# Kernel tuning notes

Measured on AMD Instinct MI355X. Metric: run time of the kernel, lower is better.

The kernel has to match this reference:

```python
import jax, jax.numpy as jnp
import numpy as np

N = 50000      # nodes
E = 800000     # edges (before self-loops)
IN_DIM = 256
HID = 32       # per-head hidden of conv1
OUT = 8        # per-head out of conv2 (mean over heads)
H = 4          # heads


def setup_inputs() -> dict:
    key = jax.random.key(0)
    k = jax.random.split(key, 8)
    x = jax.random.normal(k[0], (N, IN_DIM), dtype=jnp.float32)
    src = jax.random.randint(k[1], (E,), 0, N)
    dst = jax.random.randint(k[2], (E,), 0, N)
    # emulate remove_self_loops: perturb any accidental self-loop
    dst = jnp.where(src == dst, (dst + 1) % N, dst)
    edge_index = jnp.stack([src, dst])
    sc1 = 1.0 / np.sqrt(IN_DIM)
    W1 = jax.random.uniform(k[3], (IN_DIM, H * HID), jnp.float32, -sc1, sc1)
    att1 = jax.random.uniform(k[4], (H, HID), jnp.float32, -0.1, 0.1)
    b1 = jnp.zeros((H * HID,), jnp.float32)
    sc2 = 1.0 / np.sqrt(H * HID)
    W2 = jax.random.uniform(k[5], (H * HID, H * OUT), jnp.float32, -sc2, sc2)
    att2 = jax.random.uniform(k[6], (H, OUT), jnp.float32, -0.1, 0.1)
    b2 = jnp.zeros((OUT,), jnp.float32)
    return {"x": x, "edge_index": edge_index, "W1": W1, "att1": att1,
            "b1": b1, "W2": W2, "att2": att2, "b2": b2}


def _segment_softmax(logits, seg, num_segments):
    # logits: [E, H], seg: [E] destination ids. Every segment is non-empty
    # (self-loops added), so no -inf survives.
    m = jnp.full((num_segments, logits.shape[1]), -jnp.inf, logits.dtype)
    m = m.at[seg].max(logits)
    e = jnp.exp(logits - m[seg])
    z = jax.ops.segment_sum(e, seg, num_segments=num_segments)
    return e / (z[seg] + 1e-16)


def _oodgat_conv(x, W, att, bias, src, dst, concat):
    n = x.shape[0]
    h = (x @ W).reshape(n, att.shape[0], att.shape[1])          # [N, H, C]
    s = jax.nn.sigmoid(jnp.einsum('nhc,hc->nh', h, att))        # [N, H] node scores
    si, sj = s[dst], s[src]                                      # [E, H]
    # OODGAT similarity weight (adjust=True): agree-in-distribution term
    logits = si * sj + (1.0 - si) * (1.0 - sj)
    alpha = _segment_softmax(logits, dst, n)                     # [E, H]
    msg = h[src] * alpha[:, :, None]                             # [E, H, C]
    out = jax.ops.segment_sum(msg, dst, num_segments=n)          # [N, H, C]
    out = out.reshape(n, -1) if concat else out.mean(axis=1)
    return out + bias


def reference(x, edge_index, W1, att1, b1, W2, att2, b2):
    n = x.shape[0]
    loop = jnp.arange(n)
    src = jnp.concatenate([edge_index[0], loop])  # add_self_loops
    dst = jnp.concatenate([edge_index[1], loop])
    # eval mode: dropout (drop_input/drop_prob/drop_edge) are identity
    h = jax.nn.elu(_oodgat_conv(x, W1, att1, b1, src, dst, True))
    return _oodgat_conv(h, W2, att2, b2, src, dst, False)
```

## Files before the change

### kernel.cpp

```cpp
#include <hip/hip_runtime.h>
#include <math.h>


typedef __attribute__((ext_vector_type(8))) short bf16x8;
typedef __attribute__((ext_vector_type(4))) float f32x4;

__device__ inline ushort f2bf(float f) {
    uint u = __float_as_uint(f);
    return (ushort)((u + 0x7fffu + ((u >> 16) & 1u)) >> 16);
}
__device__ inline float bf_lo(uint u) { return __uint_as_float(u << 16); }
__device__ inline float bf_hi(uint u) { return __uint_as_float(u & 0xffff0000u); }


__global__ void count_pos_k(const int* __restrict__ dstA, int E, int ET,
                            int* __restrict__ deg, ushort* __restrict__ epos) {
    int e = blockIdx.x * blockDim.x + threadIdx.x;
    if (e >= ET) return;
    int d = (e < E) ? dstA[e] : (e - E);
    epos[e] = (ushort)atomicAdd(&deg[d], 1);
}

__global__ __launch_bounds__(256) void scan_a_k(const int* __restrict__ deg, int n,
                                                int* __restrict__ rowstart,
                                                int* __restrict__ bsum) {
    __shared__ int ts[256];
    int t = threadIdx.x;
    int idx = blockIdx.x * 1024 + t * 4;
    int4 v = make_int4(0, 0, 0, 0);
    if (idx + 3 < n) {
        v = *(const int4*)(deg + idx);
    } else {
        if (idx < n)     v.x = deg[idx];
        if (idx + 1 < n) v.y = deg[idx + 1];
        if (idx + 2 < n) v.z = deg[idx + 2];
        if (idx + 3 < n) v.w = deg[idx + 3];
    }
    int s = v.x + v.y + v.z + v.w;
    ts[t] = s;
    __syncthreads();
#pragma unroll
    for (int off = 1; off < 256; off <<= 1) {
        int u = (t >= off) ? ts[t - off] : 0;
        __syncthreads();
        ts[t] += u;
        __syncthreads();
    }
    int excl = ts[t] - s;
    int p1 = excl + v.x, p2 = p1 + v.y, p3 = p2 + v.z;
    if (idx < n)     rowstart[idx]     = excl;
    if (idx + 1 < n) rowstart[idx + 1] = p1;
    if (idx + 2 < n) rowstart[idx + 2] = p2;
    if (idx + 3 < n) rowstart[idx + 3] = p3;
    if (t == 255) bsum[blockIdx.x] = ts[255];
}

__global__ __launch_bounds__(256) void scan_b_k(const int* __restrict__ bsum, int nb,
                                                int* __restrict__ boff,
                                                int* __restrict__ totalp) {
    __shared__ int ts[256];
    int t = threadIdx.x;
    int v = (t < nb) ? bsum[t] : 0;
    ts[t] = v;
    __syncthreads();
#pragma unroll
    for (int off = 1; off < 256; off <<= 1) {
        int u = (t >= off) ? ts[t - off] : 0;
        __syncthreads();
        ts[t] += u;
        __syncthreads();
    }
    if (t < nb) boff[t] = ts[t] - v;
    if (t == nb - 1) *totalp = ts[t];
}

__global__ void scan_c_k(int* __restrict__ rowstart, const int* __restrict__ boff,
                         int n) {
    int i = blockIdx.x * blockDim.x + threadIdx.x;
    if (i < n) rowstart[i] += boff[i >> 10];
}

__global__ void scatter_k(const int* __restrict__ srcA, const int* __restrict__ dstA,
                          int E, int ET, const int* __restrict__ rowstart,
                          const ushort* __restrict__ epos,
                          ushort* __restrict__ csrc) {
    int e = blockIdx.x * blockDim.x + threadIdx.x;
    if (e >= ET) return;
    int d, s;
    if (e < E) { d = dstA[e]; s = srcA[e]; } else { d = e - E; s = e - E; }
    csrc[rowstart[d] + epos[e]] = (ushort)s;
}


__global__ void prep_wt_k(const float* __restrict__ W, ushort* __restrict__ Wt) {
    int idx = blockIdx.x * blockDim.x + threadIdx.x;
    if (idx >= 256 * 128) return;
    int k = idx >> 7, col = idx & 127;
    Wt[col * 256 + k] = f2bf(W[idx]);
}


__global__ __launch_bounds__(256) void gemm1_k(const float* __restrict__ X,
                                               const ushort* __restrict__ Wt,
                                               const float* __restrict__ ATT1,
                                               uint* __restrict__ H1b,
                                               float* __restrict__ S1, int n) {
    __shared__ __align__(16) ushort Alds[4][128][8];
    __shared__ __align__(16) ushort Blds[4][128][8];
    __shared__ float att1s[128];
    int tid = threadIdx.x;
    int wid = tid >> 6;
    int lane = tid & 63;
    int g = lane >> 4;
    int lr = lane & 15;
    int brow = blockIdx.x * 128;
    if (tid < 128) att1s[tid] = ATT1[tid];

    f32x4 acc[2][8];
#pragma unroll
    for (int rt = 0; rt < 2; ++rt)
#pragma unroll
        for (int ct = 0; ct < 8; ++ct) acc[rt][ct] = (f32x4){0.f, 0.f, 0.f, 0.f};

    for (int k0 = 0; k0 < 256; k0 += 32) {
#pragma unroll
        for (int rep = 0; rep < 2; ++rep) {
            int idx = tid + rep * 256;
            int r = idx >> 2, koct = idx & 3;
            int gr = brow + r;
            float4 a0, a1;
            if (gr < n) {
                const float* p = X + (size_t)gr * 256 + k0 + koct * 8;
                a0 = *(const float4*)p;
                a1 = *(const float4*)(p + 4);
            } else {
                a0 = a1 = make_float4(0.f, 0.f, 0.f, 0.f);
            }
            uint4 pk;
            pk.x = (uint)f2bf(a0.x) | ((uint)f2bf(a0.y) << 16);
            pk.y = (uint)f2bf(a0.z) | ((uint)f2bf(a0.w) << 16);
            pk.z = (uint)f2bf(a1.x) | ((uint)f2bf(a1.y) << 16);
            pk.w = (uint)f2bf(a1.z) | ((uint)f2bf(a1.w) << 16);
            *(uint4*)&Alds[koct][r][0] = pk;
        }
#pragma unroll
        for (int rep = 0; rep < 2; ++rep) {
            int idx = tid + rep * 256;
            int col = idx & 127, koct = idx >> 7;
            *(uint4*)&Blds[koct][col][0] =
                *(const uint4*)(Wt + (size_t)col * 256 + k0 + koct * 8);
        }
        __syncthreads();
        bf16x8 xf0 = *(bf16x8*)&Alds[g][wid * 32 + lr][0];
        bf16x8 xf1 = *(bf16x8*)&Alds[g][wid * 32 + 16 + lr][0];
#pragma unroll
        for (int ct = 0; ct < 8; ++ct) {
            bf16x8 wf = *(bf16x8*)&Blds[g][ct * 16 + lr][0];
            acc[0][ct] = __builtin_amdgcn_mfma_f32_16x16x32_bf16(wf, xf0, acc[0][ct], 0, 0, 0);
            acc[1][ct] = __builtin_amdgcn_mfma_f32_16x16x32_bf16(wf, xf1, acc[1][ct], 0, 0, 0);
        }
        __syncthreads();
    }
#pragma unroll
    for (int rt = 0; rt < 2; ++rt) {
        int row = brow + wid * 32 + rt * 16 + lr;
        if (row < n) {
#pragma unroll
            for (int ct = 0; ct < 8; ++ct) {
                uint lo = (uint)f2bf(acc[rt][ct][0]) | ((uint)f2bf(acc[rt][ct][1]) << 16);
                uint hi = (uint)f2bf(acc[rt][ct][2]) | ((uint)f2bf(acc[rt][ct][3]) << 16);
                *(uint2*)(H1b + (size_t)row * 64 + ct * 8 + g * 2) = make_uint2(lo, hi);
            }
        }
        float sc[4] = {0.f, 0.f, 0.f, 0.f};
#pragma unroll
        for (int ct = 0; ct < 8; ++ct) {
            int base = ct * 16 + g * 4;
#pragma unroll
            for (int j = 0; j < 4; ++j)
                sc[ct >> 1] = fmaf(acc[rt][ct][j], att1s[base + j], sc[ct >> 1]);
        }
#pragma unroll
        for (int h = 0; h < 4; ++h) {
            sc[h] += __shfl_xor(sc[h], 16);
            sc[h] += __shfl_xor(sc[h], 32);
        }
        if (g == 0 && row < n) {
            float4 sv;
            sv.x = 1.f / (1.f + __expf(-sc[0]));
            sv.y = 1.f / (1.f + __expf(-sc[1]));
            sv.z = 1.f / (1.f + __expf(-sc[2]));
            sv.w = 1.f / (1.f + __expf(-sc[3]));
            *(float4*)(S1 + (size_t)row * 4) = sv;
        }
    }
}


__global__ __launch_bounds__(512, 8) void conv1_k(const uint* __restrict__ H1b,
                                                  const float* __restrict__ S1,
                                                  const int* __restrict__ rowstart,
                                                  const ushort* __restrict__ csrc,
                                                  const float* __restrict__ b1,
                                                  const float* __restrict__ W2,
                                                  const float* __restrict__ ATT2,
                                                  ushort* __restrict__ H2b,
                                                  float* __restrict__ S2,
                                                  int n, int nwaves) {
    __shared__ float w2t[32][132];
    __shared__ float rowbuf[8][128];
    __shared__ float wbuf[8][64][4];
    __shared__ float att2s[32];
    int tid = threadIdx.x;
    for (int idx = tid; idx < 4096; idx += 512) {
        int k = idx >> 5, c = idx & 31;
        w2t[c][k] = W2[idx];
    }
    if (tid < 32) att2s[tid] = ATT2[tid];
    __syncthreads();

    int wid = tid >> 6;
    int lane = tid & 63;
    int hd = lane >> 4;
    int half = lane >> 5, cc2 = lane & 31;
    int gwave = blockIdx.x * 8 + wid;
    float2 b1v = *(const float2*)(b1 + lane * 2);

    for (int dst = gwave; dst < n; dst += nwaves) {
        int rs = rowstart[dst], re = rowstart[dst + 1];
        float4 si4 = *(const float4*)(S1 + (size_t)dst * 4);
        float z0 = 0.f, z1 = 0.f, z2 = 0.f, z3 = 0.f;
        float x0 = 0.f, x1 = 0.f, x2 = 0.f, x3 = 0.f;
        float y0 = 0.f, y1 = 0.f, y2 = 0.f, y3 = 0.f;

        for (int cb = rs; cb < re; cb += 64) {
            int cc = min(64, re - cb);
            int sv = 0;
            if (lane < cc) {
                sv = csrc[cb + lane];
                float4 sj = *(const float4*)(S1 + (size_t)sv * 4);
                float w0 = __expf(fmaf(si4.x, sj.x, (1.f - si4.x) * (1.f - sj.x)));
                float w1 = __expf(fmaf(si4.y, sj.y, (1.f - si4.y) * (1.f - sj.y)));
                float w2 = __expf(fmaf(si4.z, sj.z, (1.f - si4.z) * (1.f - sj.z)));
                float w3 = __expf(fmaf(si4.w, sj.w, (1.f - si4.w) * (1.f - sj.w)));
                *(float4*)&wbuf[wid][lane][0] = make_float4(w0, w1, w2, w3);
            }
            asm volatile("s_waitcnt lgkmcnt(0)" ::: "memory");
            int e = 0;
            for (; e + 7 < cc; e += 8) {
                int sA = __builtin_amdgcn_readlane(sv, e);
                int sB = __builtin_amdgcn_readlane(sv, e + 1);
                int sC = __builtin_amdgcn_readlane(sv, e + 2);
                int sD = __builtin_amdgcn_readlane(sv, e + 3);
                int sE = __builtin_amdgcn_readlane(sv, e + 4);
                int sF = __builtin_amdgcn_readlane(sv, e + 5);
                int sG = __builtin_amdgcn_readlane(sv, e + 6);
                int sH = __builtin_amdgcn_readlane(sv, e + 7);
                float wA = wbuf[wid][e][hd],     wB = wbuf[wid][e + 1][hd];
                float wC = wbuf[wid][e + 2][hd], wD = wbuf[wid][e + 3][hd];
                float wE = wbuf[wid][e + 4][hd], wF = wbuf[wid][e + 5][hd];
                float wG = wbuf[wid][e + 6][hd], wH = wbuf[wid][e + 7][hd];
                uint uA = H1b[(size_t)sA * 64 + lane];
                uint uB = H1b[(size_t)sB * 64 + lane];
                uint uC = H1b[(size_t)sC * 64 + lane];
                uint uD = H1b[(size_t)sD * 64 + lane];
                uint uE = H1b[(size_t)sE * 64 + lane];
                uint uF = H1b[(size_t)sF * 64 + lane];
                uint uG = H1b[(size_t)sG * 64 + lane];
                uint uH = H1b[(size_t)sH * 64 + lane];
                z0 += wA + wE; z1 += wB + wF; z2 += wC + wG; z3 += wD + wH;
                x0 = fmaf(wA, bf_lo(uA), x0); x1 = fmaf(wB, bf_lo(uB), x1);
                x2 = fmaf(wC, bf_lo(uC), x2); x3 = fmaf(wD, bf_lo(uD), x3);
                x0 = fmaf(wE, bf_lo(uE), x0); x1 = fmaf(wF, bf_lo(uF), x1);
                x2 = fmaf(wG, bf_lo(uG), x2); x3 = fmaf(wH, bf_lo(uH), x3);
                y0 = fmaf(wA, bf_hi(uA), y0); y1 = fmaf(wB, bf_hi(uB), y1);
                y2 = fmaf(wC, bf_hi(uC), y2); y3 = fmaf(wD, bf_hi(uD), y3);
                y0 = fmaf(wE, bf_hi(uE), y0); y1 = fmaf(wF, bf_hi(uF), y1);
                y2 = fmaf(wG, bf_hi(uG), y2); y3 = fmaf(wH, bf_hi(uH), y3);
            }
            for (; e < cc; ++e) {
                int s = __builtin_amdgcn_readlane(sv, e);
                float w = wbuf[wid][e][hd];
                uint u = H1b[(size_t)s * 64 + lane];
                z0 += w;
                x0 = fmaf(w, bf_lo(u), x0);
                y0 = fmaf(w, bf_hi(u), y0);
            }
            asm volatile("" ::: "memory");
        }
        float inv = 1.f / ((z0 + z1) + (z2 + z3) + 1e-16f);
        float r0 = ((x0 + x1) + (x2 + x3)) * inv + b1v.x;
        float r1 = ((y0 + y1) + (y2 + y3)) * inv + b1v.y;
        r0 = (r0 > 0.f) ? r0 : (__expf(r0) - 1.f);
        r1 = (r1 > 0.f) ? r1 : (__expf(r1) - 1.f);

        *(float2*)&rowbuf[wid][lane * 2] = make_float2(r0, r1);
        asm volatile("s_waitcnt lgkmcnt(0)" ::: "memory");
        const float* rb = &rowbuf[wid][half * 64];
        const float* wr = &w2t[cc2][half * 64];
        float sum = 0.f;
#pragma unroll
        for (int k = 0; k < 64; k += 4) {
            float4 rv = *(const float4*)(rb + k);
            float4 wv = *(const float4*)(wr + k);
            sum = fmaf(rv.x, wv.x, sum);
            sum = fmaf(rv.y, wv.y, sum);
            sum = fmaf(rv.z, wv.z, sum);
            sum = fmaf(rv.w, wv.w, sum);
        }
        sum += __shfl_xor(sum, 32);
        if (half == 0) H2b[(size_t)dst * 32 + cc2] = f2bf(sum);

        float v = sum * att2s[cc2];
        v += __shfl_xor(v, 1);
        v += __shfl_xor(v, 2);
        v += __shfl_xor(v, 4);
        if (half == 0 && (cc2 & 7) == 0)
            S2[dst * 4 + (cc2 >> 3)] = 1.f / (1.f + __expf(-v));
    }
}


__global__ __launch_bounds__(256, 8) void conv2_k(const uint* __restrict__ H2u,
                                                  const float* __restrict__ S,
                                                  const int* __restrict__ rowstart,
                                                  const ushort* __restrict__ csrc,
                                                  const float* __restrict__ b2,
                                                  float* __restrict__ Out,
                                                  int n, int nwaves) {
    int gwave = (int)((blockIdx.x * blockDim.x + threadIdx.x) >> 6);
    int lane = threadIdx.x & 63;
    int eslot = lane >> 4;
    int c2 = lane & 15;
    int hd = c2 >> 2;
    float2 b2v;
    b2v.x = b2[2 * (c2 & 3)];
    b2v.y = b2[2 * (c2 & 3) + 1];

    for (int dst = gwave; dst < n; dst += nwaves) {
        float si = S[dst * 4 + hd];
        float omsi = 1.f - si;
        int rs = rowstart[dst], re = rowstart[dst + 1];
        int cnt = re - rs;
        float z = 0.f, x = 0.f, y = 0.f;
        int i = eslot;
        for (; i + 4 < cnt; i += 8) {
            int s0 = csrc[rs + i];
            int s1 = csrc[rs + i + 4];
            float sj0 = S[s0 * 4 + hd];
            float sj1 = S[s1 * 4 + hd];
            uint u0 = H2u[(size_t)s0 * 16 + c2];
            uint u1 = H2u[(size_t)s1 * 16 + c2];
            float w0 = __expf(fmaf(si, sj0, omsi * (1.f - sj0)));
            float w1 = __expf(fmaf(si, sj1, omsi * (1.f - sj1)));
            z += w0 + w1;
            x = fmaf(w0, bf_lo(u0), x); x = fmaf(w1, bf_lo(u1), x);
            y = fmaf(w0, bf_hi(u0), y); y = fmaf(w1, bf_hi(u1), y);
        }
        if (i < cnt) {
            int s0 = csrc[rs + i];
            float sj0 = S[s0 * 4 + hd];
            uint u0 = H2u[(size_t)s0 * 16 + c2];
            float w0 = __expf(fmaf(si, sj0, omsi * (1.f - sj0)));
            z += w0;
            x = fmaf(w0, bf_lo(u0), x);
            y = fmaf(w0, bf_hi(u0), y);
        }
        z += __shfl_xor(z, 16); z += __shfl_xor(z, 32);
        x += __shfl_xor(x, 16); x += __shfl_xor(x, 32);
        y += __shfl_xor(y, 16); y += __shfl_xor(y, 32);
        float inv = 1.f / (z + 1e-16f);
        float r0 = x * inv, r1 = y * inv;
        r0 += __shfl_xor(r0, 4, 16); r0 += __shfl_xor(r0, 8, 16);
        r1 += __shfl_xor(r1, 4, 16); r1 += __shfl_xor(r1, 8, 16);
        if (eslot == 0 && c2 < 4) {
            float2 o = make_float2(r0 * 0.25f + b2v.x, r1 * 0.25f + b2v.y);
            *(float2*)(Out + (size_t)dst * 8 + 2 * c2) = o;
        }
    }
}


static inline size_t align16(size_t x) { return (x + 15) & ~(size_t)15; }

extern "C" void kernel_launch(void* const* d_in, const int* in_sizes, int n_in,
                              void* d_out, int out_size, void* d_ws, size_t ws_size,
                              hipStream_t stream) {
    const float* x    = (const float*)d_in[0];
    const int*   edge = (const int*)d_in[1];
    const float* W1   = (const float*)d_in[2];
    const float* att1 = (const float*)d_in[3];
    const float* b1   = (const float*)d_in[4];
    const float* W2   = (const float*)d_in[5];
    const float* att2 = (const float*)d_in[6];
    const float* b2   = (const float*)d_in[7];

    int N  = in_sizes[0] / 256;
    int E  = in_sizes[1] / 2;
    int ET = E + N;
    int NB = (N + 1023) / 1024;
    const int* srcA = edge;
    const int* dstA = edge + E;

    char* ws = (char*)d_ws;
    uint*  h1b  = (uint*)ws;   ws += align16((size_t)N * 64 * sizeof(uint));
    ushort* h2b = (ushort*)ws; ws += align16((size_t)N * 32 * sizeof(ushort));
    float* s1   = (float*)ws;  ws += align16((size_t)N * 4 * sizeof(float));
    float* s2   = (float*)ws;  ws += align16((size_t)N * 4 * sizeof(float));
    int* rowstart = (int*)ws;  ws += align16((size_t)(N + 1) * sizeof(int));
    int* deg      = (int*)ws;  ws += align16((size_t)N * sizeof(int));
    ushort* csrc  = (ushort*)ws; ws += align16((size_t)ET * sizeof(ushort));
    ushort* epos  = (ushort*)ws; ws += align16((size_t)ET * sizeof(ushort));
    int* bsum     = (int*)ws;  ws += align16((size_t)NB * sizeof(int));
    int* boff     = (int*)ws;  ws += align16((size_t)NB * sizeof(int));
    ushort* w1t   = (ushort*)ws; ws += align16((size_t)256 * 128 * sizeof(ushort));

    hipMemsetAsync(deg, 0, (size_t)N * sizeof(int), stream);

    int eb = (ET + 255) / 256;
    count_pos_k<<<eb, 256, 0, stream>>>(dstA, E, ET, deg, epos);
    scan_a_k<<<NB, 256, 0, stream>>>(deg, N, rowstart, bsum);
    scan_b_k<<<1, 256, 0, stream>>>(bsum, NB, boff, rowstart + N);
    scan_c_k<<<(N + 255) / 256, 256, 0, stream>>>(rowstart, boff, N);
    scatter_k<<<eb, 256, 0, stream>>>(srcA, dstA, E, ET, rowstart, epos, csrc);

    prep_wt_k<<<(256 * 128 + 255) / 256, 256, 0, stream>>>(W1, w1t);
    gemm1_k<<<(N + 127) / 128, 256, 0, stream>>>(x, w1t, att1, h1b, s1, N);

    int c1_blocks = 1024;
    if (c1_blocks > (N + 7) / 8) c1_blocks = (N + 7) / 8;
    int c1_waves = c1_blocks * 8;
    conv1_k<<<c1_blocks, 512, 0, stream>>>(h1b, s1, rowstart, csrc, b1, W2, att2,
                                           h2b, s2, N, c1_waves);

    int c2_blocks = 2048;
    if (c2_blocks > (N + 3) / 4) c2_blocks = (N + 3) / 4;
    int c2_waves = c2_blocks * 4;
    conv2_k<<<c2_blocks, 256, 0, stream>>>((const uint*)h2b, s2, rowstart, csrc, b2,
                                           (float*)d_out, N, c2_waves);
}
```

Before: 154.8 us.

## Vectorize CSR build kernels, use contiguous dst ranges, precompute conv2 edge weights

```diff
diff --git a/kernel.cpp b/kernel.cpp
--- a/kernel.cpp
+++ b/kernel.cpp
@@ -15,10 +15,26 @@
 
 __global__ void count_pos_k(const int* __restrict__ dstA, int E, int ET,
                             int* __restrict__ deg, ushort* __restrict__ epos) {
-    int e = blockIdx.x * blockDim.x + threadIdx.x;
-    if (e >= ET) return;
-    int d = (e < E) ? dstA[e] : (e - E);
-    epos[e] = (ushort)atomicAdd(&deg[d], 1);
+    int e4 = (blockIdx.x * blockDim.x + threadIdx.x) * 4;
+    if (e4 >= ET) return;
+    if (e4 + 3 < E) {
+        int4 d = *(const int4*)(dstA + e4);
+        ushort4 p;
+        p.x = (ushort)atomicAdd(&deg[d.x], 1);
+        p.y = (ushort)atomicAdd(&deg[d.y], 1);
+        p.z = (ushort)atomicAdd(&deg[d.z], 1);
+        p.w = (ushort)atomicAdd(&deg[d.w], 1);
+        *(ushort4*)(epos + e4) = p;
+    } else {
+#pragma unroll
+        for (int j = 0; j < 4; ++j) {
+            int e = e4 + j;
+            if (e < ET) {
+                int d = (e < E) ? dstA[e] : (e - E);
+                epos[e] = (ushort)atomicAdd(&deg[d], 1);
+            }
+        }
+    }
 }
 
 __global__ __launch_bounds__(256) void scan_a_k(const int* __restrict__ deg, int n,
@@ -84,11 +100,27 @@
                           int E, int ET, const int* __restrict__ rowstart,
                           const ushort* __restrict__ epos,
                           ushort* __restrict__ csrc) {
-    int e = blockIdx.x * blockDim.x + threadIdx.x;
-    if (e >= ET) return;
-    int d, s;
-    if (e < E) { d = dstA[e]; s = srcA[e]; } else { d = e - E; s = e - E; }
-    csrc[rowstart[d] + epos[e]] = (ushort)s;
+    int e4 = (blockIdx.x * blockDim.x + threadIdx.x) * 4;
+    if (e4 >= ET) return;
+    if (e4 + 3 < E) {
+        int4 d = *(const int4*)(dstA + e4);
+        int4 s = *(const int4*)(srcA + e4);
+        ushort4 p = *(const ushort4*)(epos + e4);
+        csrc[rowstart[d.x] + p.x] = (ushort)s.x;
+        csrc[rowstart[d.y] + p.y] = (ushort)s.y;
+        csrc[rowstart[d.z] + p.z] = (ushort)s.z;
+        csrc[rowstart[d.w] + p.w] = (ushort)s.w;
+    } else {
+#pragma unroll
+        for (int j = 0; j < 4; ++j) {
+            int e = e4 + j;
+            if (e < ET) {
+                int d, s;
+                if (e < E) { d = dstA[e]; s = srcA[e]; } else { d = e - E; s = e - E; }
+                csrc[rowstart[d] + epos[e]] = (ushort)s;
+            }
+        }
+    }
 }
 
 
@@ -224,9 +256,11 @@
     int hd = lane >> 4;
     int half = lane >> 5, cc2 = lane & 31;
     int gwave = blockIdx.x * 8 + wid;
+    int dlo = (int)((long long)gwave * n / nwaves);
+    int dhi = (int)((long long)(gwave + 1) * n / nwaves);
     float2 b1v = *(const float2*)(b1 + lane * 2);
 
-    for (int dst = gwave; dst < n; dst += nwaves) {
+    for (int dst = dlo; dst < dhi; ++dst) {
         int rs = rowstart[dst], re = rowstart[dst + 1];
         float4 si4 = *(const float4*)(S1 + (size_t)dst * 4);
         float z0 = 0.f, z1 = 0.f, z2 = 0.f, z3 = 0.f;
@@ -328,43 +362,69 @@
                                                   const float* __restrict__ b2,
                                                   float* __restrict__ Out,
                                                   int n, int nwaves) {
-    int gwave = (int)((blockIdx.x * blockDim.x + threadIdx.x) >> 6);
-    int lane = threadIdx.x & 63;
+    __shared__ float wbuf[4][64][4];
+    __shared__ ushort srcs[4][64];
+    int tid = threadIdx.x;
+    int wid = tid >> 6;
+    int lane = tid & 63;
     int eslot = lane >> 4;
     int c2 = lane & 15;
     int hd = c2 >> 2;
+    int gwave = blockIdx.x * 4 + wid;
+    int dlo = (int)((long long)gwave * n / nwaves);
+    int dhi = (int)((long long)(gwave + 1) * n / nwaves);
     float2 b2v;
     b2v.x = b2[2 * (c2 & 3)];
     b2v.y = b2[2 * (c2 & 3) + 1];
 
-    for (int dst = gwave; dst < n; dst += nwaves) {
-        float si = S[dst * 4 + hd];
-        float omsi = 1.f - si;
+    for (int dst = dlo; dst < dhi; ++dst) {
         int rs = rowstart[dst], re = rowstart[dst + 1];
-        int cnt = re - rs;
+        float4 si4 = *(const float4*)(S + (size_t)dst * 4);
         float z = 0.f, x = 0.f, y = 0.f;
-        int i = eslot;
-        for (; i + 4 < cnt; i += 8) {
-            int s0 = csrc[rs + i];
-            int s1 = csrc[rs + i + 4];
-            float sj0 = S[s0 * 4 + hd];
-            float sj1 = S[s1 * 4 + hd];
-            uint u0 = H2u[(size_t)s0 * 16 + c2];
-            uint u1 = H2u[(size_t)s1 * 16 + c2];
-            float w0 = __expf(fmaf(si, sj0, omsi * (1.f - sj0)));
-            float w1 = __expf(fmaf(si, sj1, omsi * (1.f - sj1)));
-            z += w0 + w1;
-            x = fmaf(w0, bf_lo(u0), x); x = fmaf(w1, bf_lo(u1), x);
-            y = fmaf(w0, bf_hi(u0), y); y = fmaf(w1, bf_hi(u1), y);
-        }
-        if (i < cnt) {
-            int s0 = csrc[rs + i];
-            float sj0 = S[s0 * 4 + hd];
-            uint u0 = H2u[(size_t)s0 * 16 + c2];
-            float w0 = __expf(fmaf(si, sj0, omsi * (1.f - sj0)));
-            z += w0;
-            x = fmaf(w0, bf_lo(u0), x);
-            y = fmaf(w0, bf_hi(u0), y);
+
+        for (int cb = rs; cb < re; cb += 64) {
+            int cc = min(64, re - cb);
+            if (lane < cc) {
+                int s = csrc[cb + lane];
+                float4 sj = *(const float4*)(S + (size_t)s * 4);
+                float w0 = __expf(fmaf(si4.x, sj.x, (1.f - si4.x) * (1.f - sj.x)));
+                float w1 = __expf(fmaf(si4.y, sj.y, (1.f - si4.y) * (1.f - sj.y)));
+                float w2 = __expf(fmaf(si4.z, sj.z, (1.f - si4.z) * (1.f - sj.z)));
+                float w3 = __expf(fmaf(si4.w, sj.w, (1.f - si4.w) * (1.f - sj.w)));
+                *(float4*)&wbuf[wid][lane][0] = make_float4(w0, w1, w2, w3);
+                srcs[wid][lane] = (ushort)s;
+            }
+            asm volatile("s_waitcnt lgkmcnt(0)" ::: "memory");
+            int e = 0;
+            for (; e + 7 < cc; e += 8) {
+                int sA = srcs[wid][e + eslot];
+                int sB = srcs[wid][e + 4 + eslot];
+                float wA = wbuf[wid][e + eslot][hd];
+                float wB = wbuf[wid][e + 4 + eslot][hd];
+                uint uA = H2u[(size_t)sA * 16 + c2];
+                uint uB = H2u[(size_t)sB * 16 + c2];
+                z += wA + wB;
+                x = fmaf(wA, bf_lo(uA), x); x = fmaf(wB, bf_lo(uB), x);
+                y = fmaf(wA, bf_hi(uA), y); y = fmaf(wB, bf_hi(uB), y);
+            }
+            if (e + 3 < cc) {
+                int sA = srcs[wid][e + eslot];
+                float wA = wbuf[wid][e + eslot][hd];
+                uint uA = H2u[(size_t)sA * 16 + c2];
+                z += wA;
+                x = fmaf(wA, bf_lo(uA), x);
+                y = fmaf(wA, bf_hi(uA), y);
+                e += 4;
+            }
+            if (e + eslot < cc) {
+                int sA = srcs[wid][e + eslot];
+                float wA = wbuf[wid][e + eslot][hd];
+                uint uA = H2u[(size_t)sA * 16 + c2];
+                z += wA;
+                x = fmaf(wA, bf_lo(uA), x);
+                y = fmaf(wA, bf_hi(uA), y);
+            }
+            asm volatile("" ::: "memory");
         }
         z += __shfl_xor(z, 16); z += __shfl_xor(z, 32);
         x += __shfl_xor(x, 16); x += __shfl_xor(x, 32);
@@ -417,12 +477,12 @@
 
     hipMemsetAsync(deg, 0, (size_t)N * sizeof(int), stream);
 
-    int eb = (ET + 255) / 256;
-    count_pos_k<<<eb, 256, 0, stream>>>(dstA, E, ET, deg, epos);
+    int eb4 = (ET + 1023) / 1024;
+    count_pos_k<<<eb4, 256, 0, stream>>>(dstA, E, ET, deg, epos);
     scan_a_k<<<NB, 256, 0, stream>>>(deg, N, rowstart, bsum);
     scan_b_k<<<1, 256, 0, stream>>>(bsum, NB, boff, rowstart + N);
     scan_c_k<<<(N + 255) / 256, 256, 0, stream>>>(rowstart, boff, N);
-    scatter_k<<<eb, 256, 0, stream>>>(srcA, dstA, E, ET, rowstart, epos, csrc);
+    scatter_k<<<eb4, 256, 0, stream>>>(srcA, dstA, E, ET, rowstart, epos, csrc);
 
     prep_wt_k<<<(256 * 128 + 255) / 256, 256, 0, stream>>>(W1, w1t);
     gemm1_k<<<(N + 127) / 128, 256, 0, stream>>>(x, w1t, att1, h1b, s1, N);
```

After: 165.2 us. 6.7% more time.
